# Kernel tuning notes

Hardware: AMD Instinct MI355X
Metric: run time of the kernel (lower is better)

The kernel has to match this reference:

```python
import jax, jax.numpy as jnp
import numpy as np

B, N, D = 64, 576, 384   # batch, patches (24^2, perfect square), embed_dim
K = 4096                 # n_pairs
NUM_TARGETS = 2


def setup_inputs() -> dict:
    key = jax.random.key(0)
    k1, k2, k3, k4 = jax.random.split(key, 4)
    z = jax.random.normal(k1, (B, N, D), dtype=jnp.float32)
    indices = jax.random.randint(k2, (B, K, 2), 0, N, dtype=jnp.int64)
    W = jax.random.normal(k3, (NUM_TARGETS, 2 * D), dtype=jnp.float32) * (1.0 / np.sqrt(2 * D))
    bias = jax.random.normal(k4, (NUM_TARGETS,), dtype=jnp.float32) * 0.01
    return {"z": z, "indices": indices, "W": W, "bias": bias}


def reference(z, indices, W, bias):
    b, n, d = z.shape
    _, k, _ = indices.shape
    # index_pairs: per-batch gather of both pair members -> [b, k, 2, d]
    flat_idx = indices.reshape(b, k * 2)                      # [b, 2k]
    pairs = jnp.take_along_axis(z, flat_idx[:, :, None], axis=1)  # [b, 2k, d]
    pairs = pairs.reshape(b, k, 2 * d)                        # concat pair features
    # pairwise_mlp head: Linear(2d -> num_targets)
    out = jnp.einsum('bkf,tf->bkt', pairs, W) + bias          # [b, k, num_targets]
    return out, indices
```

## Files before the change

kernel.cpp:

```cpp
#include <hip/hip_runtime.h>
#include <hip/hip_bf16.h>

#define B_ 64
#define N_ 576
#define D_ 384
#define K_ 4096

__global__ __launch_bounds__(256) void partvit_proj(const float* __restrict__ z,
                                                    const float* __restrict__ W,
                                                    float* __restrict__ y) {
    const int wave = (blockIdx.x * blockDim.x + threadIdx.x) >> 6;
    const int lane = threadIdx.x & 63;
    if (wave >= B_ * N_) return;

    const float* zr = z + (size_t)wave * D_;
    float a0 = 0.f, a1 = 0.f, a2 = 0.f, a3 = 0.f;
#pragma unroll
    for (int j = 0; j < D_ / 64; ++j) {
        const int c = lane + 64 * j;
        const float x = zr[c];
        a0 += x * W[c];
        a1 += x * W[768 + c];
        a2 += x * W[384 + c];
        a3 += x * W[1152 + c];
    }
#pragma unroll
    for (int off = 32; off > 0; off >>= 1) {
        a0 += __shfl_xor(a0, off);
        a1 += __shfl_xor(a1, off);
        a2 += __shfl_xor(a2, off);
        a3 += __shfl_xor(a3, off);
    }
    if (lane == 0) {
        float4 v;
        v.x = a0; v.y = a1; v.z = a2; v.w = a3;
        *reinterpret_cast<float4*>(y + (size_t)wave * 4) = v;
    }
}

__global__ __launch_bounds__(256) void partvit_gather(const int* __restrict__ idx,
                                                      const float* __restrict__ y,
                                                      const float* __restrict__ bias,
                                                      float* __restrict__ out,
                                                      float* __restrict__ idx_out) {
    const int t = blockIdx.x * blockDim.x + threadIdx.x;
    if (t >= B_ * K_) return;
    const int b = t >> 12;

    const int2 p = reinterpret_cast<const int2*>(idx)[t];
    const float* yb = y + (size_t)b * N_ * 4;

    const float2 y0 = *reinterpret_cast<const float2*>(yb + (size_t)p.x * 4);
    const float2 y1 = *reinterpret_cast<const float2*>(yb + (size_t)p.y * 4 + 2);

    const float b0 = bias[0], b1 = bias[1];

    float2 o;
    o.x = y0.x + y1.x + b0;
    o.y = y0.y + y1.y + b1;
    reinterpret_cast<float2*>(out)[t] = o;

    float2 io;
    io.x = (float)p.x;
    io.y = (float)p.y;
    reinterpret_cast<float2*>(idx_out)[t] = io;
}

extern "C" void kernel_launch(void* const* d_in, const int* in_sizes, int n_in,
                              void* d_out, int out_size, void* d_ws, size_t ws_size,
                              hipStream_t stream) {
    const float* z    = (const float*)d_in[0];
    const int*   idx  = (const int*)d_in[1];
    const float* W    = (const float*)d_in[2];
    const float* bias = (const float*)d_in[3];

    float* out     = (float*)d_out;
    float* idx_out = (float*)d_out + (size_t)B_ * K_ * 2;
    float* y       = (float*)d_ws;

    const int rows = B_ * N_;
    partvit_proj<<<(rows + 3) / 4, 256, 0, stream>>>(z, W, y);

    const int pairs = B_ * K_;
    partvit_gather<<<(pairs + 255) / 256, 256, 0, stream>>>(idx, y, bias, out, idx_out);
}
```

Measured before the change: 20.32 us.

## Vectorize projection kernel with float4 loads, register-cached weights, persistent grid

The projection kernel now has each half-wave handle one row with float4 loads, so a wave covers two rows. The four weight slices are loaded into registers once per thread and reused across rows. A fixed grid of 1024 blocks loops over row pairs instead of launching one wave per row. This is meant to cut per-row weight reloads, scalar loads and launch tail cost, in exchange for more register pressure and a shorter 5-step shuffle reduction.

```diff
diff --git a/kernel.cpp b/kernel.cpp
--- a/kernel.cpp
+++ b/kernel.cpp
@@ -9,32 +9,50 @@
 __global__ __launch_bounds__(256) void partvit_proj(const float* __restrict__ z,
                                                     const float* __restrict__ W,
                                                     float* __restrict__ y) {
-    const int wave = (blockIdx.x * blockDim.x + threadIdx.x) >> 6;
+    const int wid  = (blockIdx.x * blockDim.x + threadIdx.x) >> 6;
     const int lane = threadIdx.x & 63;
-    if (wave >= B_ * N_) return;
+    const int h = lane >> 5;
+    const int s = lane & 31;
 
-    const float* zr = z + (size_t)wave * D_;
-    float a0 = 0.f, a1 = 0.f, a2 = 0.f, a3 = 0.f;
+    const float4* Wq = reinterpret_cast<const float4*>(W);
+    const float4* zq = reinterpret_cast<const float4*>(z);
+
+    float4 w0a[3], w1a[3], w0b[3], w1b[3];
 #pragma unroll
-    for (int j = 0; j < D_ / 64; ++j) {
-        const int c = lane + 64 * j;
-        const float x = zr[c];
-        a0 += x * W[c];
-        a1 += x * W[768 + c];
-        a2 += x * W[384 + c];
-        a3 += x * W[1152 + c];
+    for (int m = 0; m < 3; ++m) {
+        const int c4 = s * 3 + m;
+        w0a[m] = Wq[c4];
+        w0b[m] = Wq[96 + c4];
+        w1a[m] = Wq[192 + c4];
+        w1b[m] = Wq[288 + c4];
     }
+
+    const int npairs = (B_ * N_) / 2;
+    const int nwaves = (gridDim.x * blockDim.x) >> 6;
+    for (int pid = wid; pid < npairs; pid += nwaves) {
+        const int row = pid * 2 + h;
+        const float4* zr = zq + (size_t)row * 96 + s * 3;
+        float a0 = 0.f, a1 = 0.f, a2 = 0.f, a3 = 0.f;
 #pragma unroll
-    for (int off = 32; off > 0; off >>= 1) {
-        a0 += __shfl_xor(a0, off);
-        a1 += __shfl_xor(a1, off);
-        a2 += __shfl_xor(a2, off);
-        a3 += __shfl_xor(a3, off);
-    }
-    if (lane == 0) {
-        float4 v;
-        v.x = a0; v.y = a1; v.z = a2; v.w = a3;
-        *reinterpret_cast<float4*>(y + (size_t)wave * 4) = v;
+        for (int m = 0; m < 3; ++m) {
+            const float4 v = zr[m];
+            a0 += v.x * w0a[m].x + v.y * w0a[m].y + v.z * w0a[m].z + v.w * w0a[m].w;
+            a1 += v.x * w1a[m].x + v.y * w1a[m].y + v.z * w1a[m].z + v.w * w1a[m].w;
+            a2 += v.x * w0b[m].x + v.y * w0b[m].y + v.z * w0b[m].z + v.w * w0b[m].w;
+            a3 += v.x * w1b[m].x + v.y * w1b[m].y + v.z * w1b[m].z + v.w * w1b[m].w;
+        }
+#pragma unroll
+        for (int off = 16; off > 0; off >>= 1) {
+            a0 += __shfl_xor(a0, off);
+            a1 += __shfl_xor(a1, off);
+            a2 += __shfl_xor(a2, off);
+            a3 += __shfl_xor(a3, off);
+        }
+        if (s == 0) {
+            float4 v;
+            v.x = a0; v.y = a1; v.z = a2; v.w = a3;
+            reinterpret_cast<float4*>(y)[row] = v;
+        }
     }
 }
 
@@ -78,8 +96,7 @@
     float* idx_out = (float*)d_out + (size_t)B_ * K_ * 2;
     float* y       = (float*)d_ws;
 
-    const int rows = B_ * N_;
-    partvit_proj<<<(rows + 3) / 4, 256, 0, stream>>>(z, W, y);
+    partvit_proj<<<1024, 256, 0, stream>>>(z, W, y);
 
     const int pairs = B_ * K_;
     partvit_gather<<<(pairs + 255) / 256, 256, 0, stream>>>(idx, y, bias, out, idx_out);
```

New measurement: 19.47 us. 4.2% less time.
